# Optimization experiments

Hardware: AMD Instinct MI355X
Metric: run time of the kernel (lower is better)

## Reference

```python
import jax, jax.numpy as jnp
import numpy as np
import math

B, T, C, H, S_CACHE = 2, 1024, 2048, 16, 1024
DK = C // H


def setup_inputs() -> dict:
    key = jax.random.key(0)
    ks = jax.random.split(key, 7)
    x = jax.random.normal(ks[0], (B, T, C), dtype=jnp.float32)
    cache_k = jax.random.normal(ks[1], (B, H, S_CACHE, DK), dtype=jnp.float32)
    cache_v = jax.random.normal(ks[2], (B, H, S_CACHE, DK), dtype=jnp.float32)
    scale = 0.02
    Wq = jax.random.normal(ks[3], (C, C), dtype=jnp.float32) * scale
    Wk = jax.random.normal(ks[4], (C, C), dtype=jnp.float32) * scale
    Wv = jax.random.normal(ks[5], (C, C), dtype=jnp.float32) * scale
    Wo = jax.random.normal(ks[6], (C, C), dtype=jnp.float32) * scale
    return {"x": x, "cache_k": cache_k, "cache_v": cache_v,
            "Wq": Wq, "Wk": Wk, "Wv": Wv, "Wo": Wo}


def reference(x, cache_k, cache_v, Wq, Wk, Wv, Wo):
    b, t, c = x.shape
    h = cache_k.shape[1]
    dk = c // h
    # nn.Linear: y = x @ W.T  (weights stored [out, in])
    Q = (x @ Wq.T).reshape(b, t, h, dk).transpose(0, 2, 1, 3)  # [B,H,T,dk]
    K = (x @ Wk.T).reshape(b, t, h, dk).transpose(0, 2, 1, 3)
    V = (x @ Wv.T).reshape(b, t, h, dk).transpose(0, 2, 1, 3)
    K = jnp.concatenate([cache_k, K], axis=2)  # [B,H,S,dk]
    V = jnp.concatenate([cache_v, V], axis=2)
    s = K.shape[2]
    scores = jnp.einsum('bhtd,bhsd->bhts', Q, K) / math.sqrt(dk)
    # faithful to the source: mask = tril(ones(T, S)) (no cache offset); T==1 -> all ones
    if t == 1:
        mask = jnp.ones((1, s), dtype=jnp.float32)
    else:
        mask = jnp.tril(jnp.ones((t, s), dtype=jnp.float32))
    scores = jnp.where(mask == 0, jnp.float32(-jnp.inf), scores)
    attn = jax.nn.softmax(scores, axis=-1)
    out = jnp.einsum('bhts,bhsd->bhtd', attn, V)
    out = out.transpose(0, 2, 1, 3).reshape(b, t, c)
    return (out @ Wo.T, K, V)
```

## Files before the change

kernel.cpp:

```cpp
#include <hip/hip_runtime.h>

typedef unsigned short u16;
typedef short bf16x8 __attribute__((ext_vector_type(8)));
typedef float f32x4 __attribute__((ext_vector_type(4)));
typedef unsigned short u16x4 __attribute__((ext_vector_type(4)));

#define AS1 __attribute__((address_space(1)))
#define AS3 __attribute__((address_space(3)))

__device__ __forceinline__ u16 f2bf(float f) {
    unsigned u = __float_as_uint(f);
    u += 0x7fff + ((u >> 16) & 1);
    return (u16)(u >> 16);
}

__device__ __forceinline__ void gld16(const void* g, void* l) {
    __builtin_amdgcn_global_load_lds((const AS1 void*)g, (AS3 void*)l, 16, 0, 0);
}

__global__ void convall_kernel(const float* __restrict__ x,  const float* __restrict__ wq,
                               const float* __restrict__ wk, const float* __restrict__ wv,
                               const float* __restrict__ wo,
                               u16* __restrict__ xb, u16* __restrict__ wqkv, u16* __restrict__ wob) {
    int t = blockIdx.x * 256 + threadIdx.x;
    const float* srcs[5] = { x, wq, wk, wv, wo };
    u16* dsts[5] = { xb, wqkv, wqkv + 4194304, wqkv + 8388608, wob };
#pragma unroll
    for (int r = 0; r < 5; r++) {
        f32x4 v = ((const f32x4*)srcs[r])[t];
        u16x4 o = { f2bf(v.x), f2bf(v.y), f2bf(v.z), f2bf(v.w) };
        ((u16x4*)dsts[r])[t] = o;
    }
}

__global__ void cachek_kernel(const float* __restrict__ ck, float* __restrict__ kout,
                              u16* __restrict__ kcb) {
    const int n4 = (2 * 16 * 1024 * 128) / 4;
    int i = blockIdx.x * 256 + threadIdx.x;
    int stride = gridDim.x * 256;
    for (; i < n4; i += stride) {
        f32x4 v = ((const f32x4*)ck)[i];
        int bh = i >> 15;
        ((f32x4*)kout)[i + bh * 32768] = v;
        u16x4 o = { f2bf(v.x), f2bf(v.y), f2bf(v.z), f2bf(v.w) };
        ((u16x4*)kcb)[i] = o;
    }
}

__global__ void vtrans_kernel(const float* __restrict__ cv, float* __restrict__ vout,
                              u16* __restrict__ vtb) {
    __shared__ u16 tile[64 * 65];
    const int bh = blockIdx.x;
    const int s0 = blockIdx.y * 64;
    const int d0 = blockIdx.z * 64;
    const float* src = cv + (size_t)bh * 1024 * 128;
#pragma unroll
    for (int i = 0; i < 16; i++) {
        int e = i * 256 + threadIdx.x;
        int sr = e >> 6, dc = e & 63;
        float v = src[(size_t)(s0 + sr) * 128 + d0 + dc];
        vout[((size_t)bh * 2048 + s0 + sr) * 128 + d0 + dc] = v;
        tile[sr * 65 + dc] = f2bf(v);
    }
    __syncthreads();
    u16* dst = vtb + (size_t)bh * 128 * 1024;
#pragma unroll
    for (int i = 0; i < 16; i++) {
        int e = i * 256 + threadIdx.x;
        int dr = e >> 6, sc = e & 63;
        dst[(size_t)(d0 + dr) * 1024 + s0 + sc] = tile[sc * 65 + dr];
    }
}

template <int MODE>
__global__ __launch_bounds__(256) void gemm_bt_kernel(
    const u16* __restrict__ A, const u16* __restrict__ Bm,
    u16* __restrict__ qout, float* __restrict__ kout, float* __restrict__ vout,
    float* __restrict__ cout) {
    __shared__ u16 As[64 * 64];
    __shared__ u16 Bs[128 * 64];
    const int tid = threadIdx.x;
    const int lane = tid & 63, wv = tid >> 6;
    const int wn = wv * 32;
    const int m0 = blockIdx.y * 64, n0 = blockIdx.x * 128;
    const int frow = lane & 15, fq = lane >> 4;
    const int swz = frow & 7;

    f32x4 acc[4][2];
#pragma unroll
    for (int a = 0; a < 4; a++)
#pragma unroll
        for (int b = 0; b < 2; b++) acc[a][b] = (f32x4){0.f, 0.f, 0.f, 0.f};

    for (int k0 = 0; k0 < 2048; k0 += 64) {
        __syncthreads();
#pragma unroll
        for (int i = 0; i < 2; i++) {
            int L = i * 256 + tid;
            int row = L >> 3;
            int c = (L & 7) ^ (row & 7);
            gld16(A + (size_t)(m0 + row) * 2048 + k0 + c * 8, As + i * 2048 + wv * 512);
        }
#pragma unroll
        for (int i = 0; i < 4; i++) {
            int L = i * 256 + tid;
            int row = L >> 3;
            int c = (L & 7) ^ (row & 7);
            gld16(Bm + (size_t)(n0 + row) * 2048 + k0 + c * 8, Bs + i * 2048 + wv * 512);
        }
        __syncthreads();
#pragma unroll
        for (int kk = 0; kk < 2; kk++) {
            bf16x8 aF[4], bF[2];
#pragma unroll
            for (int f = 0; f < 4; f++)
                aF[f] = *(const bf16x8*)(As + (f * 16 + frow) * 64 + ((kk * 4 + fq) ^ swz) * 8);
#pragma unroll
            for (int f = 0; f < 2; f++)
                bF[f] = *(const bf16x8*)(Bs + (wn + f * 16 + frow) * 64 + ((kk * 4 + fq) ^ swz) * 8);
#pragma unroll
            for (int fm = 0; fm < 4; fm++)
#pragma unroll
                for (int fn = 0; fn < 2; fn++)
                    acc[fm][fn] = __builtin_amdgcn_mfma_f32_16x16x32_bf16(aF[fm], bF[fn], acc[fm][fn], 0, 0, 0);
        }
    }

#pragma unroll
    for (int fm = 0; fm < 4; fm++) {
#pragma unroll
        for (int fn = 0; fn < 2; fn++) {
#pragma unroll
            for (int r = 0; r < 4; r++) {
                int m = m0 + fm * 16 + fq * 4 + r;
                int n = n0 + wn + fn * 16 + frow;
                float v = acc[fm][fn][r];
                if (MODE == 0) {
                    int b = m >> 10, t = m & 1023;
                    int sect = n >> 11, nn = n & 2047;
                    int h = nn >> 7, d = nn & 127;
                    size_t bh = (size_t)(b * 16 + h);
                    if (sect == 0)
                        qout[(bh * 1024 + t) * 128 + d] = f2bf(v * 0.08838834764831843f);
                    else if (sect == 1)
                        kout[(bh * 2048 + 1024 + t) * 128 + d] = v;
                    else
                        vout[(bh * 2048 + 1024 + t) * 128 + d] = v;
                } else {
                    cout[(size_t)m * 2048 + n] = v;
                }
            }
        }
    }
}

__global__ __launch_bounds__(256) void attn_kernel(
    const u16* __restrict__ Qb, const u16* __restrict__ Kcb,
    const u16* __restrict__ Vtb, u16* __restrict__ AOb,
    float* __restrict__ PO, float* __restrict__ PML) {
    __shared__ u16 Qs[64 * 128];
    __shared__ u16 Ks[64 * 128];
    __shared__ u16 Vs[128 * 64];
    __shared__ u16 Ps[64 * 64];
    const int bid = blockIdx.x;
    int bh, qi, st_begin, st_end, cidx;
    bool partial;
    if (bid < 512) {
        qi = 15 - (bid >> 6);
        int j = bid & 63;
        bh = j >> 1;
        int c = j & 1;
        int n = qi + 1, h0 = (n + 1) >> 1;
        st_begin = c ? h0 : 0;
        st_end = c ? n : h0;
        partial = true;
        cidx = c * 256 + bh * 8 + (qi - 8);
    } else {
        int j = bid - 512;
        qi = 7 - (j >> 5);
        bh = j & 31;
        st_begin = 0; st_end = qi + 1;
        partial = false; cidx = 0;
    }
    const int t0 = qi * 64;
    const int tid = threadIdx.x, lane = tid & 63, wv = tid >> 6;
    const int row_w = wv * 16;
    const int frow = lane & 15, fq = lane >> 4;
    const int swz = frow & 7;

    const u16* Qg = Qb + ((size_t)bh * 1024 + t0) * 128;
#pragma unroll
    for (int i = 0; i < 4; i++) {
        int L = i * 256 + tid;
        int row = L >> 4;
        int c = (L & 15) ^ (row & 7);
        gld16(Qg + row * 128 + c * 8, Qs + i * 2048 + wv * 512);
    }

    float mrow[4], lrow[4];
    f32x4 Oacc[8];
#pragma unroll
    for (int r = 0; r < 4; r++) { mrow[r] = -1e30f; lrow[r] = 0.f; }
#pragma unroll
    for (int fd = 0; fd < 8; fd++) Oacc[fd] = (f32x4){0.f, 0.f, 0.f, 0.f};

    for (int st = st_begin; st < st_end; st++) {
        int s0 = st * 64;
        __syncthreads();
        const u16* Kg = Kcb + ((size_t)bh * 1024 + s0) * 128;
#pragma unroll
        for (int i = 0; i < 4; i++) {
            int L = i * 256 + tid;
            int row = L >> 4;
            int c = (L & 15) ^ (row & 7);
            gld16(Kg + row * 128 + c * 8, Ks + i * 2048 + wv * 512);
        }
        const u16* Vg = Vtb + (size_t)bh * 131072 + s0;
#pragma unroll
        for (int i = 0; i < 4; i++) {
            int L = i * 256 + tid;
            int row = L >> 3;
            int c = (L & 7) ^ (row & 7);
            gld16(Vg + row * 1024 + c * 8, Vs + i * 2048 + wv * 512);
        }
        __syncthreads();

        f32x4 S[4];
#pragma unroll
        for (int fn = 0; fn < 4; fn++) S[fn] = (f32x4){0.f, 0.f, 0.f, 0.f};
#pragma unroll
        for (int kk = 0; kk < 4; kk++) {
            bf16x8 aF = *(const bf16x8*)(Qs + (row_w + frow) * 128 + ((kk * 4 + fq) ^ swz) * 8);
#pragma unroll
            for (int fn = 0; fn < 4; fn++) {
                bf16x8 bF = *(const bf16x8*)(Ks + (fn * 16 + frow) * 128 + ((kk * 4 + fq) ^ swz) * 8);
                S[fn] = __builtin_amdgcn_mfma_f32_16x16x32_bf16(aF, bF, S[fn], 0, 0, 0);
            }
        }

        if (st == qi) {
#pragma unroll
            for (int fn = 0; fn < 4; fn++)
#pragma unroll
                for (int r = 0; r < 4; r++) {
                    int t = t0 + row_w + fq * 4 + r;
                    int s = s0 + fn * 16 + frow;
                    if (s > t) S[fn][r] = -1e30f;
                }
        }

#pragma unroll
        for (int r = 0; r < 4; r++) {
            float mx = fmaxf(fmaxf(S[0][r], S[1][r]), fmaxf(S[2][r], S[3][r]));
            mx = fmaxf(mx, __shfl_xor(mx, 1));
            mx = fmaxf(mx, __shfl_xor(mx, 2));
            mx = fmaxf(mx, __shfl_xor(mx, 4));
            mx = fmaxf(mx, __shfl_xor(mx, 8));
            float mnew = fmaxf(mrow[r], mx);
            float alpha = __expf(mrow[r] - mnew);
            float rs = 0.f;
#pragma unroll
            for (int fn = 0; fn < 4; fn++) {
                float p = __expf(S[fn][r] - mnew);
                S[fn][r] = p;
                rs += p;
            }
            rs += __shfl_xor(rs, 1);
            rs += __shfl_xor(rs, 2);
            rs += __shfl_xor(rs, 4);
            rs += __shfl_xor(rs, 8);
            mrow[r] = mnew;
            lrow[r] = lrow[r] * alpha + rs;
#pragma unroll
            for (int fd = 0; fd < 8; fd++) Oacc[fd][r] *= alpha;
        }

#pragma unroll
        for (int fn = 0; fn < 4; fn++)
#pragma unroll
            for (int r = 0; r < 4; r++) {
                int pr = row_w + fq * 4 + r;
                int c = fn * 2 + (frow >> 3);
                Ps[pr * 64 + ((c ^ (pr & 7)) * 8) + (frow & 7)] = f2bf(S[fn][r]);
            }

#pragma unroll
        for (int ks = 0; ks < 2; ks++) {
            int rr = row_w + frow;
            bf16x8 aP = *(const bf16x8*)(Ps + rr * 64 + ((ks * 4 + fq) ^ (rr & 7)) * 8);
#pragma unroll
            for (int fd = 0; fd < 8; fd++) {
                int vr = fd * 16 + frow;
                bf16x8 bV = *(const bf16x8*)(Vs + vr * 64 + ((ks * 4 + fq) ^ (vr & 7)) * 8);
                Oacc[fd] = __builtin_amdgcn_mfma_f32_16x16x32_bf16(aP, bV, Oacc[fd], 0, 0, 0);
            }
        }
    }

    if (partial) {
        float* Od = PO + (size_t)cidx * 8192;
#pragma unroll
        for (int r = 0; r < 4; r++) {
            int row = row_w + fq * 4 + r;
#pragma unroll
            for (int fd = 0; fd < 8; fd++)
                Od[row * 128 + fd * 16 + frow] = Oacc[fd][r];
        }
        if (frow == 0) {
#pragma unroll
            for (int r = 0; r < 4; r++) {
                int row = row_w + fq * 4 + r;
                PML[cidx * 128 + row * 2] = mrow[r];
                PML[cidx * 128 + row * 2 + 1] = lrow[r];
            }
        }
    } else {
        const int b = bh >> 4, h = bh & 15;
#pragma unroll
        for (int r = 0; r < 4; r++) {
            float rl = 1.0f / lrow[r];
            int t = t0 + row_w + fq * 4 + r;
#pragma unroll
            for (int fd = 0; fd < 8; fd++) {
                int col = h * 128 + fd * 16 + frow;
                AOb[((size_t)b * 1024 + t) * 2048 + col] = f2bf(Oacc[fd][r] * rl);
            }
        }
    }
}

__global__ __launch_bounds__(256) void attn_merge_kernel(
    const float* __restrict__ PO, const float* __restrict__ PML, u16* __restrict__ AOb) {
    const int idx = blockIdx.x;
    const int bh = idx >> 3, qi = 8 + (idx & 7);
    const int t0 = qi * 64;
    const int b = bh >> 4, h = bh & 15;
    const int tid = threadIdx.x;
    const int row = tid >> 2, cg = tid & 3;
    const float* O0 = PO + (size_t)idx * 8192;
    const float* O1 = PO + (size_t)(256 + idx) * 8192;
    float m0 = PML[idx * 128 + row * 2],        l0 = PML[idx * 128 + row * 2 + 1];
    float m1 = PML[(256 + idx) * 128 + row * 2], l1 = PML[(256 + idx) * 128 + row * 2 + 1];
    float mm = fmaxf(m0, m1);
    float w0 = __expf(m0 - mm), w1 = __expf(m1 - mm);
    float inv = 1.0f / (l0 * w0 + l1 * w1);
    u16* dst = AOb + ((size_t)b * 1024 + t0 + row) * 2048 + h * 128 + cg * 32;
#pragma unroll
    for (int j = 0; j < 8; j++) {
        f32x4 a = *(const f32x4*)(O0 + row * 128 + cg * 32 + j * 4);
        f32x4 c = *(const f32x4*)(O1 + row * 128 + cg * 32 + j * 4);
        u16x4 o = { f2bf((a.x * w0 + c.x * w1) * inv), f2bf((a.y * w0 + c.y * w1) * inv),
                    f2bf((a.z * w0 + c.z * w1) * inv), f2bf((a.w * w0 + c.w * w1) * inv) };
        *(u16x4*)(dst + j * 4) = o;
    }
}

extern "C" void kernel_launch(void* const* d_in, const int* in_sizes, int n_in,
                              void* d_out, int out_size, void* d_ws, size_t ws_size,
                              hipStream_t stream) {
    const float* x  = (const float*)d_in[0];
    const float* ck = (const float*)d_in[1];
    const float* cv = (const float*)d_in[2];
    const float* Wq = (const float*)d_in[3];
    const float* Wk = (const float*)d_in[4];
    const float* Wv = (const float*)d_in[5];
    const float* Wo = (const float*)d_in[6];

    float* out  = (float*)d_out;
    float* Kout = out + 4194304;
    float* Vout = out + 12582912;

    u16* xb   = (u16*)d_ws;
    u16* Wqkv = xb + 4194304;
    u16* Wob  = Wqkv + 12582912;
    u16* Qb   = Wob + 4194304;
    u16* Kcb  = Qb + 4194304;
    u16* Vtb  = Kcb + 4194304;
    u16* AOb  = Vtb + 4194304;
    float* PO  = (float*)Wqkv;
    float* PML = PO + 4194304;

    convall_kernel<<<4096, 256, 0, stream>>>(x, Wq, Wk, Wv, Wo, xb, Wqkv, Wob);
    cachek_kernel<<<1024, 256, 0, stream>>>(ck, Kout, Kcb);
    vtrans_kernel<<<dim3(32, 16, 2), 256, 0, stream>>>(cv, Vout, Vtb);

    gemm_bt_kernel<0><<<dim3(48, 32), 256, 0, stream>>>(xb, Wqkv, Qb, Kout, Vout, nullptr);
    attn_kernel<<<768, 256, 0, stream>>>(Qb, Kcb, Vtb, AOb, PO, PML);
    attn_merge_kernel<<<256, 256, 0, stream>>>(PO, PML, AOb);
    gemm_bt_kernel<1><<<dim3(16, 32), 256, 0, stream>>>(AOb, Wob, nullptr, nullptr, nullptr, out);
}
```

Before: 326.3 us.

## Rewrite QKV GEMM as 256x256 double-buffered ping-pong kernel with setprio

Replaces the 64x128-tile QKV projection GEMM with a 512-thread kernel that computes 256x256 tiles. It double-buffers LDS loads issued through global_load_lds and interleaves the staged loads with four MFMA phases per k-step, gated by barriers and s_setprio. It also raises wave priority around the MFMA sections of the attention kernel. The aim is more data reuse per tile and overlap of memory traffic with matrix math. The cost is 128KB of LDS per block, heavy register use, and only 192 blocks for the GEMM, which may underfill the device.

Measured after the change: 324.9 us. Within noise of the previous version (-0.4%).

```diff
diff --git a/kernel.cpp b/kernel.cpp
--- a/kernel.cpp
+++ b/kernel.cpp
@@ -72,11 +72,143 @@
     }
 }
 
-template <int MODE>
-__global__ __launch_bounds__(256) void gemm_bt_kernel(
+#define PH_COMPUTE(MO, NO, BREG) \
+    __builtin_amdgcn_s_barrier(); \
+    asm volatile("s_waitcnt lgkmcnt(0)" ::: "memory"); \
+    __builtin_amdgcn_sched_barrier(0); \
+    __builtin_amdgcn_s_setprio(1); \
+    _Pragma("unroll") \
+    for (int mf = 0; mf < 4; mf++) { \
+        _Pragma("unroll") \
+        for (int nf = 0; nf < 2; nf++) { \
+            _Pragma("unroll") \
+            for (int kk = 0; kk < 2; kk++) \
+                acc[MO + mf][NO + nf] = __builtin_amdgcn_mfma_f32_16x16x32_bf16( \
+                    aF[mf][kk], BREG[nf][kk], acc[MO + mf][NO + nf], 0, 0, 0); \
+        } \
+    } \
+    __builtin_amdgcn_s_setprio(0); \
+    __builtin_amdgcn_s_barrier();
+
+#define HALF(P, S1, S2, S3, S4, VM) \
+    { \
+        _Pragma("unroll") \
+        for (int mf = 0; mf < 4; mf++) \
+            _Pragma("unroll") \
+            for (int kk = 0; kk < 2; kk++) aF[mf][kk] = rdA(P, mf, kk); \
+        _Pragma("unroll") \
+        for (int nf = 0; nf < 2; nf++) \
+            _Pragma("unroll") \
+            for (int kk = 0; kk < 2; kk++) bLo[nf][kk] = rdB(P, nf, kk); \
+        S1; \
+        PH_COMPUTE(0, 0, bLo) \
+        _Pragma("unroll") \
+        for (int nf = 0; nf < 2; nf++) \
+            _Pragma("unroll") \
+            for (int kk = 0; kk < 2; kk++) bHi[nf][kk] = rdB(P, 2 + nf, kk); \
+        S2; \
+        PH_COMPUTE(0, 2, bHi) \
+        _Pragma("unroll") \
+        for (int mf = 0; mf < 4; mf++) \
+            _Pragma("unroll") \
+            for (int kk = 0; kk < 2; kk++) aF[mf][kk] = rdA(P, 4 + mf, kk); \
+        S3; \
+        PH_COMPUTE(4, 2, bHi) \
+        S4; \
+        VM; \
+        PH_COMPUTE(4, 0, bLo) \
+    }
+
+__global__ __launch_bounds__(512, 2) void gemm_qkv_kernel(
     const u16* __restrict__ A, const u16* __restrict__ Bm,
-    u16* __restrict__ qout, float* __restrict__ kout, float* __restrict__ vout,
-    float* __restrict__ cout) {
+    u16* __restrict__ qout, float* __restrict__ kout, float* __restrict__ vout) {
+    __shared__ u16 Ab[2][16384];
+    __shared__ u16 Bb[2][16384];
+    const int tid = threadIdx.x;
+    const int lane = tid & 63, wv8 = tid >> 6;
+    const int wrow = (wv8 >> 2) * 128;
+    const int wcol = (wv8 & 3) * 64;
+    const int m0 = blockIdx.y * 256, n0 = blockIdx.x * 256;
+    const int frow = lane & 15, fq = lane >> 4;
+    const int swz = frow & 7;
+
+    f32x4 acc[8][4];
+#pragma unroll
+    for (int a = 0; a < 8; a++)
+#pragma unroll
+        for (int b = 0; b < 4; b++) acc[a][b] = (f32x4){0.f, 0.f, 0.f, 0.f};
+
+    auto stA = [&](int kt, int half) {
+        u16* dst = &Ab[kt & 1][half * 8192];
+#pragma unroll
+        for (int j = 0; j < 2; j++) {
+            int L = j * 512 + tid;
+            int row = L >> 3, c = (L & 7) ^ (row & 7);
+            gld16(A + (size_t)(m0 + half * 128 + row) * 2048 + kt * 64 + c * 8,
+                  dst + j * 4096 + wv8 * 512);
+        }
+    };
+    auto stB = [&](int kt, int half) {
+        u16* dst = &Bb[kt & 1][half * 8192];
+#pragma unroll
+        for (int j = 0; j < 2; j++) {
+            int L = j * 512 + tid;
+            int row = L >> 3, c = (L & 7) ^ (row & 7);
+            gld16(Bm + (size_t)(n0 + half * 128 + row) * 2048 + kt * 64 + c * 8,
+                  dst + j * 4096 + wv8 * 512);
+        }
+    };
+    auto rdA = [&](int p, int mf, int kk) {
+        int r = wrow + mf * 16 + frow;
+        return *(const bf16x8*)(&Ab[p][r * 64 + (((kk << 2) + fq) ^ swz) * 8]);
+    };
+    auto rdB = [&](int p, int nf, int kk) {
+        int r = wcol + nf * 16 + frow;
+        return *(const bf16x8*)(&Bb[p][r * 64 + (((kk << 2) + fq) ^ swz) * 8]);
+    };
+
+    bf16x8 aF[4][2], bLo[2][2], bHi[2][2];
+
+    stA(0, 0); stA(0, 1); stB(0, 0); stB(0, 1); stB(1, 0); stB(1, 1);
+    asm volatile("s_waitcnt vmcnt(4)" ::: "memory");
+    __builtin_amdgcn_s_barrier();
+
+    for (int u = 0; u < 30; u += 2) {
+        HALF(0, stA(u + 1, 0), stA(u + 1, 1), stB(u + 2, 0), stB(u + 2, 1),
+             asm volatile("s_waitcnt vmcnt(4)" ::: "memory"))
+        HALF(1, stA(u + 2, 0), stA(u + 2, 1), stB(u + 3, 0), stB(u + 3, 1),
+             asm volatile("s_waitcnt vmcnt(4)" ::: "memory"))
+    }
+    HALF(0, stA(31, 0), stA(31, 1), (void)0, (void)0,
+         asm volatile("s_waitcnt vmcnt(0)" ::: "memory"))
+    HALF(1, (void)0, (void)0, (void)0, (void)0, (void)0)
+
+#pragma unroll
+    for (int fm = 0; fm < 8; fm++) {
+#pragma unroll
+        for (int fn = 0; fn < 4; fn++) {
+#pragma unroll
+            for (int r = 0; r < 4; r++) {
+                int m = m0 + wrow + fm * 16 + fq * 4 + r;
+                int n = n0 + wcol + fn * 16 + frow;
+                float v = acc[fm][fn][r];
+                int b = m >> 10, t = m & 1023;
+                int sect = n >> 11, nn = n & 2047;
+                int h = nn >> 7, d = nn & 127;
+                size_t bh = (size_t)(b * 16 + h);
+                if (sect == 0)
+                    qout[(bh * 1024 + t) * 128 + d] = f2bf(v * 0.08838834764831843f);
+                else if (sect == 1)
+                    kout[(bh * 2048 + 1024 + t) * 128 + d] = v;
+                else
+                    vout[(bh * 2048 + 1024 + t) * 128 + d] = v;
+            }
+        }
+    }
+}
+
+__global__ __launch_bounds__(256) void gemm_out_kernel(
+    const u16* __restrict__ A, const u16* __restrict__ Bm, float* __restrict__ cout) {
     __shared__ u16 As[64 * 64];
     __shared__ u16 Bs[128 * 64];
     const int tid = threadIdx.x;
@@ -134,21 +266,7 @@
             for (int r = 0; r < 4; r++) {
                 int m = m0 + fm * 16 + fq * 4 + r;
                 int n = n0 + wn + fn * 16 + frow;
-                float v = acc[fm][fn][r];
-                if (MODE == 0) {
-                    int b = m >> 10, t = m & 1023;
-                    int sect = n >> 11, nn = n & 2047;
-                    int h = nn >> 7, d = nn & 127;
-                    size_t bh = (size_t)(b * 16 + h);
-                    if (sect == 0)
-                        qout[(bh * 1024 + t) * 128 + d] = f2bf(v * 0.08838834764831843f);
-                    else if (sect == 1)
-                        kout[(bh * 2048 + 1024 + t) * 128 + d] = v;
-                    else
-                        vout[(bh * 2048 + 1024 + t) * 128 + d] = v;
-                } else {
-                    cout[(size_t)m * 2048 + n] = v;
-                }
+                cout[(size_t)m * 2048 + n] = acc[fm][fn][r];
             }
         }
     }
@@ -228,6 +346,7 @@
         f32x4 S[4];
 #pragma unroll
         for (int fn = 0; fn < 4; fn++) S[fn] = (f32x4){0.f, 0.f, 0.f, 0.f};
+        __builtin_amdgcn_s_setprio(1);
 #pragma unroll
         for (int kk = 0; kk < 4; kk++) {
             bf16x8 aF = *(const bf16x8*)(Qs + (row_w + frow) * 128 + ((kk * 4 + fq) ^ swz) * 8);
@@ -237,6 +356,7 @@
                 S[fn] = __builtin_amdgcn_mfma_f32_16x16x32_bf16(aF, bF, S[fn], 0, 0, 0);
             }
         }
+        __builtin_amdgcn_s_setprio(0);
 
         if (st == qi) {
 #pragma unroll
@@ -284,6 +404,7 @@
                 Ps[pr * 64 + ((c ^ (pr & 7)) * 8) + (frow & 7)] = f2bf(S[fn][r]);
             }
 
+        __builtin_amdgcn_s_setprio(1);
 #pragma unroll
         for (int ks = 0; ks < 2; ks++) {
             int rr = row_w + frow;
@@ -295,6 +416,7 @@
                 Oacc[fd] = __builtin_amdgcn_mfma_f32_16x16x32_bf16(aP, bV, Oacc[fd], 0, 0, 0);
             }
         }
+        __builtin_amdgcn_s_setprio(0);
     }
 
     if (partial) {
@@ -384,8 +506,8 @@
     cachek_kernel<<<1024, 256, 0, stream>>>(ck, Kout, Kcb);
     vtrans_kernel<<<dim3(32, 16, 2), 256, 0, stream>>>(cv, Vout, Vtb);
 
-    gemm_bt_kernel<0><<<dim3(48, 32), 256, 0, stream>>>(xb, Wqkv, Qb, Kout, Vout, nullptr);
+    gemm_qkv_kernel<<<dim3(24, 8), 512, 0, stream>>>(xb, Wqkv, Qb, Kout, Vout);
     attn_kernel<<<768, 256, 0, stream>>>(Qb, Kcb, Vtb, AOb, PO, PML);
     attn_merge_kernel<<<256, 256, 0, stream>>>(PO, PML, AOb);
-    gemm_bt_kernel<1><<<dim3(16, 32), 256, 0, stream>>>(AOb, Wob, nullptr, nullptr, nullptr, out);
-}
+    gemm_out_kernel<<<dim3(16, 32), 256, 0, stream>>>(AOb, Wob, out);
+}
```
